# Kernel optimization log

Hardware: AMD Instinct MI355X
Metric: run time of the kernel (lower is better)

Reference implementation:

```python
import jax, jax.numpy as jnp
import numpy as np

B, NLB, NPB, SDIM = 128, 32, 160, 256  # complexes, ligand atoms, pocket CAs, scalar dim


def _uniform(key, shape, fan_in):
    # kaiming_uniform_(a=sqrt(5)) -> U(-1/sqrt(fan_in), 1/sqrt(fan_in))
    bound = 1.0 / np.sqrt(fan_in)
    return jax.random.uniform(key, shape, jnp.float32, -bound, bound)


def setup_inputs() -> dict:
    key = jax.random.key(0)
    k1, k2, k3, k4, k5 = jax.random.split(key, 5)
    NL, NP = B * NLB, B * NPB
    # block-diagonal cross adjacency: every ligand atom paired with every pocket CA
    # of the same complex (same as (batch_ligand[:,None]==batch_pocket[None,:]).nonzero().T)
    l = np.repeat(np.arange(NL, dtype=np.int32), NPB)
    p = (np.arange(B, dtype=np.int32)[:, None, None] * NPB
         + np.zeros((1, NLB, 1), dtype=np.int32)
         + np.arange(NPB, dtype=np.int32)[None, None, :]).reshape(-1)
    return {
        "s_ligand": jax.random.normal(k1, (NL, SDIM), jnp.float32),
        "s_pocket": jax.random.normal(k2, (NP, SDIM), jnp.float32),
        "l": jnp.asarray(l),
        "p": jnp.asarray(p),
        "W1": _uniform(k3, (SDIM // 2, SDIM), SDIM),
        "b1": jnp.zeros((SDIM // 2,), jnp.float32),
        "W2": _uniform(k4, (SDIM // 4, SDIM // 2), SDIM // 2),
        "b2": jnp.zeros((SDIM // 4,), jnp.float32),
        "W3": _uniform(k5, (1, SDIM // 4), SDIM // 4),
        "b3": jnp.zeros((1,), jnp.float32),
    }


def reference(s_ligand, s_pocket, l, p, W1, b1, W2, b2, W3, b3):
    # gather cross-pair embeddings and sum: s[e] = s_ligand[l[e]] + s_pocket[p[e]]
    s = s_ligand[l] + s_pocket[p]                      # [E, sdim]
    h = jax.nn.silu(s @ W1.T + b1)                     # [E, sdim/2]
    h = jax.nn.silu(h @ W2.T + b2)                     # [E, sdim/4]
    out = jax.nn.relu(h @ W3.T + b3)                   # [E, 1]
    return out.squeeze(-1)                             # [E]
```

## Files before the change

### kernel.cpp

```cpp
#include <hip/hip_runtime.h>
#include <hip/hip_bf16.h>


#define B_CPLX   128
#define NLB      32
#define NPB      160
#define SDIM     256
#define H1DIM    128
#define NL_TOT   (B_CPLX * NLB)
#define NP_TOT   (B_CPLX * NPB)
#define NROWS    (NL_TOT + NP_TOT)
#define E_TOT    (B_CPLX * NLB * NPB)

#define W1_LDS_STRIDE 264
#define JT_CHUNK 16
#define ZP_STRIDE 132

typedef __bf16 bf16x8 __attribute__((ext_vector_type(8)));
typedef unsigned short ushortx8 __attribute__((ext_vector_type(8)));
typedef unsigned short ushortx4 __attribute__((ext_vector_type(4)));
typedef unsigned uintx4 __attribute__((ext_vector_type(4)));
typedef float f32x4 __attribute__((ext_vector_type(4)));

__device__ __forceinline__ unsigned short f2bf(float f) {
    unsigned u = __builtin_bit_cast(unsigned, f);
    u += 0x7FFFu + ((u >> 16) & 1u);
    return (unsigned short)(u >> 16);
}

__device__ __forceinline__ unsigned perm_hi16u(unsigned u0, unsigned u1) {
    return __builtin_amdgcn_perm(u1, u0, 0x07060302u);
}

__device__ __forceinline__ unsigned pack2_rhu(float x0, float x1) {
    unsigned u0 = __builtin_bit_cast(unsigned, x0) + 0x8000u;
    unsigned u1 = __builtin_bit_cast(unsigned, x1) + 0x8000u;
    return perm_hi16u(u0, u1);
}

__device__ __forceinline__ bf16x8 pack8_rhu(const float* x) {
    uintx4 h;
#pragma unroll
    for (int j = 0; j < 4; ++j) h[j] = pack2_rhu(x[2 * j], x[2 * j + 1]);
    return __builtin_bit_cast(bf16x8, h);
}

__device__ __forceinline__ void pack_split(const float* x, bf16x8& hi, bf16x8& lo) {
    uintx4 h, l;
#pragma unroll
    for (int j = 0; j < 4; ++j) {
        float x0 = x[2 * j], x1 = x[2 * j + 1];
        unsigned u0 = __builtin_bit_cast(unsigned, x0);
        unsigned u1 = __builtin_bit_cast(unsigned, x1);
        h[j] = perm_hi16u(u0, u1);
        float hf0 = __builtin_bit_cast(float, u0 & 0xFFFF0000u);
        float hf1 = __builtin_bit_cast(float, u1 & 0xFFFF0000u);
        l[j] = pack2_rhu(x0 - hf0, x1 - hf1);
    }
    hi = __builtin_bit_cast(bf16x8, h);
    lo = __builtin_bit_cast(bf16x8, l);
}

__device__ __forceinline__ float fast_silu(float x) {
    return x * __builtin_amdgcn_rcpf(1.0f + __expf(-x));
}

__device__ __forceinline__ float rowsum16(float s) {
    int b;
    b = __builtin_bit_cast(int, s);
    b = __builtin_amdgcn_update_dpp(b, b, 0x121, 0xF, 0xF, false);
    s += __builtin_bit_cast(float, b);
    b = __builtin_bit_cast(int, s);
    b = __builtin_amdgcn_update_dpp(b, b, 0x122, 0xF, 0xF, false);
    s += __builtin_bit_cast(float, b);
    b = __builtin_bit_cast(int, s);
    b = __builtin_amdgcn_update_dpp(b, b, 0x124, 0xF, 0xF, false);
    s += __builtin_bit_cast(float, b);
    b = __builtin_bit_cast(int, s);
    b = __builtin_amdgcn_update_dpp(b, b, 0x128, 0xF, 0xF, false);
    s += __builtin_bit_cast(float, b);
    return s;
}

__global__ __launch_bounds__(256) void proj_kernel(
    const float* __restrict__ s_lig, const float* __restrict__ s_poc,
    const float* __restrict__ W1,    const float* __restrict__ b1,
    float* __restrict__ Z)
{
    __shared__ unsigned short w1s[64 * W1_LDS_STRIDE];

    const int tid  = threadIdx.x;
    const int tg   = blockIdx.x >> 1;
    const int half = blockIdx.x & 1;

    {
        const f32x4* w4 = (const f32x4*)(W1 + (size_t)half * 64 * SDIM);
#pragma unroll
        for (int r = 0; r < 2; ++r) {
            f32x4 t[8];
#pragma unroll
            for (int s = 0; s < 8; ++s) t[s] = w4[tid + (r * 8 + s) * 256];
#pragma unroll
            for (int s = 0; s < 8; ++s) {
                const int u = tid + (r * 8 + s) * 256;
                const int n = u >> 6;
                const int k4 = u & 63;
                ushortx4 us;
#pragma unroll
                for (int j = 0; j < 4; ++j) us[j] = f2bf(t[s][j]);
                *(ushortx4*)(&w1s[n * W1_LDS_STRIDE + k4 * 4]) = us;
            }
        }
    }
    __syncthreads();

    const int lane = tid & 63;
    const int widx = tid >> 6;
    const int c    = lane & 15;
    const int q    = lane >> 4;
    const int tile = tg * 4 + widx;
    const int row  = tile * 16 + c;

    const float* src = (row < NL_TOT) ? (s_lig + (size_t)row * SDIM)
                                      : (s_poc + (size_t)(row - NL_TOT) * SDIM);

    f32x4 acc[4];
#pragma unroll
    for (int nt = 0; nt < 4; ++nt) acc[nt] = (f32x4){0.f, 0.f, 0.f, 0.f};

#pragma unroll
    for (int ks = 0; ks < 8; ++ks) {
        const int k0 = ks * 32 + q * 8;
        f32x4 xa = *reinterpret_cast<const f32x4*>(src + k0);
        f32x4 xb = *reinterpret_cast<const f32x4*>(src + k0 + 4);
        float xv[8] = {xa[0], xa[1], xa[2], xa[3], xb[0], xb[1], xb[2], xb[3]};
        bf16x8 ahi, alo;
        pack_split(xv, ahi, alo);
        bf16x8 bfrag[4];
#pragma unroll
        for (int nt = 0; nt < 4; ++nt)
            bfrag[nt] = *reinterpret_cast<const bf16x8*>(
                &w1s[(nt * 16 + c) * W1_LDS_STRIDE + k0]);
#pragma unroll
        for (int nt = 0; nt < 4; ++nt)
            acc[nt] = __builtin_amdgcn_mfma_f32_16x16x32_bf16(ahi, bfrag[nt], acc[nt], 0, 0, 0);
#pragma unroll
        for (int nt = 0; nt < 4; ++nt)
            acc[nt] = __builtin_amdgcn_mfma_f32_16x16x32_bf16(alo, bfrag[nt], acc[nt], 0, 0, 0);
    }

    const int mb = tile * 16 + q * 4;
#pragma unroll
    for (int nt = 0; nt < 4; ++nt) {
        const int n = half * 64 + nt * 16 + c;
        const float bias = b1[n];
#pragma unroll
        for (int r = 0; r < 4; ++r) {
            const int m = mb + r;
            float v = acc[nt][r];
            if (m < NL_TOT) v += bias;
            Z[(size_t)m * H1DIM + n] = v;
        }
    }
}

__global__ __launch_bounds__(256) void edge_kernel(
    const float* __restrict__ Z,
    const float* __restrict__ W2, const float* __restrict__ b2,
    const float* __restrict__ W3, const float* __restrict__ b3,
    float* __restrict__ out)
{
    __shared__ float zp[JT_CHUNK * ZP_STRIDE];
    __shared__ unsigned short w2s[16 * 64 * 8];

    const int tid = threadIdx.x;
    const int bid = blockIdx.x;
    const int b   = bid / 20;
    const int rem = bid - b * 20;
    const int jt  = rem >> 1;
    const int ih  = rem & 1;

    {
        const float* zpg = Z + (size_t)(NL_TOT + b * NPB + jt * JT_CHUNK) * H1DIM;
#pragma unroll
        for (int s = 0; s < 2; ++s) {
            const int u   = tid + s * 256;
            const int row = u >> 5;
            const int c4  = u & 31;
            f32x4 v = *(const f32x4*)(zpg + (size_t)row * H1DIM + c4 * 4);
            *(f32x4*)(&zp[row * ZP_STRIDE + c4 * 4]) = v;
        }
    }

    {
#pragma unroll
        for (int s = 0; s < 4; ++s) {
            const int slot   = tid + s * 256;
            const int lane_s = slot & 63;
            const int chunk  = slot >> 6;
            const int nt     = chunk >> 2;
            const int ks     = chunk & 3;
            const int n      = nt * 16 + (lane_s & 15);
            const int k0     = ks * 32 + (lane_s >> 4) * 8;
            const float* wsrc = W2 + (size_t)n * H1DIM + k0;
            f32x4 wa = *(const f32x4*)wsrc;
            f32x4 wb = *(const f32x4*)(wsrc + 4);
            float wv[8] = {wa[0], wa[1], wa[2], wa[3], wb[0], wb[1], wb[2], wb[3]};
            ushortx8 us;
#pragma unroll
            for (int j = 0; j < 8; ++j) us[j] = f2bf(wv[j]);
            *(ushortx8*)(&w2s[slot * 8]) = us;
        }
    }

    const int lane = tid & 63;
    const int widx = tid >> 6;
    const int c    = lane & 15;
    const int q    = lane >> 4;

    float b2f[4], w3f[4];
#pragma unroll
    for (int nt = 0; nt < 4; ++nt) {
        b2f[nt] = b2[nt * 16 + c];
        w3f[nt] = W3[nt * 16 + c];
    }
    const float b3v = b3[0];

    __syncthreads();

    const float* lgbase = Z + (size_t)(b * NLB) * H1DIM;
    const float* prow   = &zp[c * ZP_STRIDE];
    const unsigned short* wbase = &w2s[lane * 8];

    const int a0 = ih * 16 + widx * 4;

    f32x4 lgA[4][2], lgB[4][2];
    {
        const float* lr0 = lgbase + (size_t)a0 * H1DIM;
#pragma unroll
        for (int ks = 0; ks < 4; ++ks) {
            const int k0 = ks * 32 + q * 8;
            lgA[ks][0] = *(const f32x4*)(lr0 + k0);
            lgA[ks][1] = *(const f32x4*)(lr0 + k0 + 4);
            lgB[ks][0] = *(const f32x4*)(lr0 + H1DIM + k0);
            lgB[ks][1] = *(const f32x4*)(lr0 + H1DIM + k0 + 4);
        }
    }

#pragma unroll
    for (int pair = 0; pair < 2; ++pair) {
        const int i0 = a0 + pair * 2;

        f32x4 acc0[4], acc1[4];
#pragma unroll
        for (int nt = 0; nt < 4; ++nt) {
            const float bb = b2f[nt];
            acc0[nt] = (f32x4){bb, bb, bb, bb};
            acc1[nt] = (f32x4){bb, bb, bb, bb};
        }

#pragma unroll
        for (int ks = 0; ks < 4; ++ks) {
            const int k0 = ks * 32 + q * 8;
            bf16x8 bfr[4];
#pragma unroll
            for (int nt = 0; nt < 4; ++nt)
                bfr[nt] = *(const bf16x8*)(wbase + (nt * 4 + ks) * 512);
            f32x4 pa = *(const f32x4*)(prow + k0);
            f32x4 pb = *(const f32x4*)(prow + k0 + 4);
            float hv0[8], hv1[8];
#pragma unroll
            for (int j = 0; j < 4; ++j) {
                hv0[j]     = fast_silu(pa[j] + lgA[ks][0][j]);
                hv0[4 + j] = fast_silu(pb[j] + lgA[ks][1][j]);
                hv1[j]     = fast_silu(pa[j] + lgB[ks][0][j]);
                hv1[4 + j] = fast_silu(pb[j] + lgB[ks][1][j]);
            }
            bf16x8 a0f = pack8_rhu(hv0);
            bf16x8 a1f = pack8_rhu(hv1);
#pragma unroll
            for (int nt = 0; nt < 4; ++nt)
                acc0[nt] = __builtin_amdgcn_mfma_f32_16x16x32_bf16(a0f, bfr[nt], acc0[nt], 0, 0, 0);
#pragma unroll
            for (int nt = 0; nt < 4; ++nt)
                acc1[nt] = __builtin_amdgcn_mfma_f32_16x16x32_bf16(a1f, bfr[nt], acc1[nt], 0, 0, 0);
        }

        {
            const float* lrn = lgbase + (size_t)(i0 + 2) * H1DIM;
#pragma unroll
            for (int ks = 0; ks < 4; ++ks) {
                const int k0 = ks * 32 + q * 8;
                lgA[ks][0] = *(const f32x4*)(lrn + k0);
                lgA[ks][1] = *(const f32x4*)(lrn + k0 + 4);
                lgB[ks][0] = *(const f32x4*)(lrn + H1DIM + k0);
                lgB[ks][1] = *(const f32x4*)(lrn + H1DIM + k0 + 4);
            }
        }

#pragma unroll
        for (int at = 0; at < 2; ++at) {
            const f32x4* A = at ? acc1 : acc0;
            float s0 = 0.f, s1 = 0.f, s2 = 0.f, s3 = 0.f;
#pragma unroll
            for (int nt = 0; nt < 4; ++nt) {
                s0 += fast_silu(A[nt][0]) * w3f[nt];
                s1 += fast_silu(A[nt][1]) * w3f[nt];
                s2 += fast_silu(A[nt][2]) * w3f[nt];
                s3 += fast_silu(A[nt][3]) * w3f[nt];
            }
            s0 = rowsum16(s0);
            s1 = rowsum16(s1);
            s2 = rowsum16(s2);
            s3 = rowsum16(s3);
            if (c < 4) {
                float v = (c == 0) ? s0 : (c == 1) ? s1 : (c == 2) ? s2 : s3;
                const int e0 = (b * NLB + i0 + at) * NPB + jt * JT_CHUNK;
                out[e0 + q * 4 + c] = fmaxf(v + b3v, 0.0f);
            }
        }
    }
}

extern "C" void kernel_launch(void* const* d_in, const int* in_sizes, int n_in,
                              void* d_out, int out_size, void* d_ws, size_t ws_size,
                              hipStream_t stream)
{
    const float* s_lig = (const float*)d_in[0];
    const float* s_poc = (const float*)d_in[1];
    const float* W1    = (const float*)d_in[4];
    const float* b1    = (const float*)d_in[5];
    const float* W2    = (const float*)d_in[6];
    const float* b2    = (const float*)d_in[7];
    const float* W3    = (const float*)d_in[8];
    const float* b3    = (const float*)d_in[9];

    float* Z = (float*)d_ws;

    hipLaunchKernelGGL(proj_kernel, dim3(NROWS / 16 / 4 * 2), dim3(256), 0, stream,
                       s_lig, s_poc, W1, b1, Z);
    hipLaunchKernelGGL(edge_kernel, dim3(B_CPLX * 20), dim3(256), 0, stream,
                       Z, W2, b2, W3, b3, (float*)d_out);
}
```

Baseline: 138.5 us.

## Factor silu exponential into per-ligand and per-pocket precomputed terms

Uses exp(-(a+b)) = exp(-a)*exp(-b) so the per-edge sigmoid no longer evaluates a transcendental. The block precomputes exp(-x) for its pocket rows into registers and for its ligand rows into a new LDS buffer, then each edge needs only an FMA and a reciprocal. This removes the per-edge exp from the silu hot loop. In exchange it adds LDS traffic and registers, and the product of exponentials can overflow to inf for large negative inputs, which changes behaviour where the old form stayed finite.

Result: no change. 138.8 us (+0.2%).

```diff
diff --git a/kernel.cpp b/kernel.cpp
--- a/kernel.cpp
+++ b/kernel.cpp
@@ -15,6 +15,7 @@
 #define W1_LDS_STRIDE 264
 #define JT_CHUNK 16
 #define ZP_STRIDE 132
+#define LOG2E 1.44269504088896340736f
 
 typedef __bf16 bf16x8 __attribute__((ext_vector_type(8)));
 typedef unsigned short ushortx8 __attribute__((ext_vector_type(8)));
@@ -61,8 +62,12 @@
     lo = __builtin_bit_cast(bf16x8, l);
 }
 
+__device__ __forceinline__ float exp2_raw(float x) {
+    return __builtin_amdgcn_exp2f(x);
+}
+
 __device__ __forceinline__ float fast_silu(float x) {
-    return x * __builtin_amdgcn_rcpf(1.0f + __expf(-x));
+    return x * __builtin_amdgcn_rcpf(1.0f + exp2_raw(-LOG2E * x));
 }
 
 __device__ __forceinline__ float rowsum16(float s) {
@@ -171,6 +176,7 @@
     float* __restrict__ out)
 {
     __shared__ float zp[JT_CHUNK * ZP_STRIDE];
+    __shared__ float epl[16 * ZP_STRIDE];
     __shared__ unsigned short w2s[16 * 64 * 8];
 
     const int tid = threadIdx.x;
@@ -189,6 +195,21 @@
             const int c4  = u & 31;
             f32x4 v = *(const f32x4*)(zpg + (size_t)row * H1DIM + c4 * 4);
             *(f32x4*)(&zp[row * ZP_STRIDE + c4 * 4]) = v;
+        }
+    }
+
+    {
+        const float* zlg = Z + (size_t)(b * NLB + ih * 16) * H1DIM;
+#pragma unroll
+        for (int s = 0; s < 2; ++s) {
+            const int u   = tid + s * 256;
+            const int row = u >> 5;
+            const int c4  = u & 31;
+            f32x4 v = *(const f32x4*)(zlg + (size_t)row * H1DIM + c4 * 4);
+            f32x4 e;
+#pragma unroll
+            for (int j = 0; j < 4; ++j) e[j] = exp2_raw(-LOG2E * v[j]);
+            *(f32x4*)(&epl[row * ZP_STRIDE + c4 * 4]) = e;
         }
     }
 
@@ -232,7 +253,21 @@
     const float* prow   = &zp[c * ZP_STRIDE];
     const unsigned short* wbase = &w2s[lane * 8];
 
+    f32x4 ep[4][2];
+#pragma unroll
+    for (int ks = 0; ks < 4; ++ks) {
+        const int k0 = ks * 32 + q * 8;
+        f32x4 a = *(const f32x4*)(prow + k0);
+        f32x4 bb = *(const f32x4*)(prow + k0 + 4);
+#pragma unroll
+        for (int j = 0; j < 4; ++j) {
+            ep[ks][0][j] = exp2_raw(-LOG2E * a[j]);
+            ep[ks][1][j] = exp2_raw(-LOG2E * bb[j]);
+        }
+    }
+
     const int a0 = ih * 16 + widx * 4;
+    const int la = widx * 4;
 
     f32x4 lgA[4][2], lgB[4][2];
     {
@@ -250,6 +285,8 @@
 #pragma unroll
     for (int pair = 0; pair < 2; ++pair) {
         const int i0 = a0 + pair * 2;
+        const float* elA = &epl[(la + pair * 2) * ZP_STRIDE];
+        const float* elB = elA + ZP_STRIDE;
 
         f32x4 acc0[4], acc1[4];
 #pragma unroll
@@ -268,13 +305,21 @@
                 bfr[nt] = *(const bf16x8*)(wbase + (nt * 4 + ks) * 512);
             f32x4 pa = *(const f32x4*)(prow + k0);
             f32x4 pb = *(const f32x4*)(prow + k0 + 4);
+            f32x4 eA0 = *(const f32x4*)(elA + k0);
+            f32x4 eA1 = *(const f32x4*)(elA + k0 + 4);
+            f32x4 eB0 = *(const f32x4*)(elB + k0);
+            f32x4 eB1 = *(const f32x4*)(elB + k0 + 4);
             float hv0[8], hv1[8];
 #pragma unroll
             for (int j = 0; j < 4; ++j) {
-                hv0[j]     = fast_silu(pa[j] + lgA[ks][0][j]);
-                hv0[4 + j] = fast_silu(pb[j] + lgA[ks][1][j]);
-                hv1[j]     = fast_silu(pa[j] + lgB[ks][0][j]);
-                hv1[4 + j] = fast_silu(pb[j] + lgB[ks][1][j]);
+                float xA0 = pa[j] + lgA[ks][0][j];
+                float xA1 = pb[j] + lgA[ks][1][j];
+                float xB0 = pa[j] + lgB[ks][0][j];
+                float xB1 = pb[j] + lgB[ks][1][j];
+                hv0[j]     = xA0 * __builtin_amdgcn_rcpf(fmaf(ep[ks][0][j], eA0[j], 1.0f));
+                hv0[4 + j] = xA1 * __builtin_amdgcn_rcpf(fmaf(ep[ks][1][j], eA1[j], 1.0f));
+                hv1[j]     = xB0 * __builtin_amdgcn_rcpf(fmaf(ep[ks][0][j], eB0[j], 1.0f));
+                hv1[4 + j] = xB1 * __builtin_amdgcn_rcpf(fmaf(ep[ks][1][j], eB1[j], 1.0f));
             }
             bf16x8 a0f = pack8_rhu(hv0);
             bf16x8 a1f = pack8_rhu(hv1);
```
